# Optimization experiments

Hardware: AMD Instinct MI355X
Metric: run time of the kernel (lower is better)

## Reference

```python
import jax, jax.numpy as jnp
import numpy as np

EMA_DECAY = 0.99
LAPLACE_EPS = 1e-7
PERPLEXITY_EPS = 1e-10
COMMIT_COEF = 0.25


def setup_inputs() -> dict:
    key = jax.random.key(0)
    k1, k2, k3, k4 = jax.random.split(key, 4)
    B, C, T, H, W = 8, 256, 4, 32, 32
    n_codes = 2048
    z = jax.random.normal(k1, (B, C, T, H, W), dtype=jnp.float32)
    embeddings = jax.random.normal(k2, (n_codes, C), dtype=jnp.float32)
    N = jnp.ones((n_codes,), dtype=jnp.float32)  # state after _init_embeddings
    z_avg = jax.random.normal(k3, (n_codes, C), dtype=jnp.float32)
    k_rand = jax.random.normal(k4, (n_codes, C), dtype=jnp.float32)  # stand-in for randperm restart rows
    return {"z": z, "embeddings": embeddings, "N": N, "z_avg": z_avg, "k_rand": k_rand}


def reference(z, embeddings, N, z_avg, k_rand):
    b, c, t, h, w = z.shape
    n_codes = embeddings.shape[0]
    # rearrange 'b c t h w -> (b t h w) c'
    flat = jnp.transpose(z, (0, 2, 3, 4, 1)).reshape(-1, c)  # [Ntok, c]
    d2 = ((flat * flat).sum(axis=1, keepdims=True)
          - 2.0 * (flat @ embeddings.T)
          + (embeddings * embeddings).sum(axis=1)[None, :])  # [Ntok, n_codes]
    idx = jnp.argmin(d2, axis=1)  # [Ntok] int
    quant_flat = embeddings[idx]  # gather, [Ntok, c]
    # back to [b, c, t, h, w] (the double-rearrange in the torch code is a net permute back)
    quant = jnp.transpose(quant_flat.reshape(b, t, h, w, c), (0, 4, 1, 2, 3))
    commitment_loss = COMMIT_COEF * jnp.mean((z - jax.lax.stop_gradient(quant)) ** 2)
    embeddings_st = jax.lax.stop_gradient(quant - z) + z  # straight-through
    # EMA codebook update (one-hot scatter expressed as segment_sum)
    ones = jnp.ones(flat.shape[0], dtype=flat.dtype)
    counts = jax.ops.segment_sum(ones, idx, num_segments=n_codes)          # n_total
    encode_sum = jax.ops.segment_sum(flat, idx, num_segments=n_codes)      # [n_codes, c]
    new_N = N * EMA_DECAY + (1.0 - EMA_DECAY) * counts
    new_z_avg = z_avg * EMA_DECAY + (1.0 - EMA_DECAY) * encode_sum
    n = new_N.sum()
    weights = (new_N + LAPLACE_EPS) / (n + n_codes * LAPLACE_EPS) * n
    new_embeddings = new_z_avg / weights[:, None]
    usage = (new_N[:, None] >= 1.0).astype(flat.dtype)
    new_embeddings = new_embeddings * usage + k_rand * (1.0 - usage)
    # perplexity
    avg_probs = counts / flat.shape[0]
    perplexity = jnp.exp(-jnp.sum(avg_probs * jnp.log(avg_probs + PERPLEXITY_EPS)))
    encodings = idx.reshape(b, t, h, w)
    return embeddings_st, encodings, commitment_loss, perplexity, new_embeddings, new_N, new_z_avg
```

## Files before the change

kernel.cpp:

```cpp
#include <hip/hip_runtime.h>
#include <math.h>

#define NCODES 2048
#define CDIM   256
#define SPAT   4096
#define NTOK   32768
#define XSTR   260
#define EPI_TOK 16

#define ETILE    32
#define HALFCODE 1024
#define NTILES   (HALFCODE / ETILE)

typedef _Float16 half8  __attribute__((ext_vector_type(8)));
typedef float    f32x4  __attribute__((ext_vector_type(4)));

#define WS_ENORM  0
#define WS_COUNTS 2048
#define WS_LOSS   4096
#define WS_N      4097
#define WS_ESUM   4100
#define WS_IDX    528388
#define WS_OFF    561156
#define WS_CUR    563204
#define WS_SORT   565252
#define WS_SCODE  598020
#define WS_CAND   630788
#define WS_E16    761860
#define WS_XH     1024004

#define O_QUANT 0
#define O_ENC   8388608
#define O_LOSS  8421376
#define O_PERP  8421377
#define O_EMB   8421378
#define O_NN    8945666
#define O_ZAVG  8947714

__device__ inline void gl_lds16(const void* g, void* l) {
    __builtin_amdgcn_global_load_lds(
        (const __attribute__((address_space(1))) void*)g,
        (__attribute__((address_space(3))) void*)l, 16, 0, 0);
}

__device__ inline unsigned umn(unsigned a, unsigned b) { return a < b ? a : b; }
__device__ inline unsigned umx(unsigned a, unsigned b) { return a > b ? a : b; }
__device__ inline unsigned shflx16(unsigned v, int off) {
    return (unsigned)__shfl_xor((int)v, off, 16);
}

__global__ void k_ecvt(const float* __restrict__ emb, float* __restrict__ ws) {
    const int tid  = threadIdx.x;
    const int code = (blockIdx.x << 3) + (tid >> 5);
    const int cg   = tid & 31;
    const float* src = emb + (size_t)code * CDIM + (cg << 3);
    const float4 f0 = *(const float4*)src;
    const float4 f1 = *(const float4*)(src + 4);
    half8 h = { (_Float16)f0.x, (_Float16)f0.y, (_Float16)f0.z, (_Float16)f0.w,
                (_Float16)f1.x, (_Float16)f1.y, (_Float16)f1.z, (_Float16)f1.w };
    char* dst = (char*)(ws + WS_E16) + (size_t)code * 512 + ((cg ^ (code & 7)) << 4);
    *(half8*)dst = h;
    float s = f0.x * f0.x + f0.y * f0.y + f0.z * f0.z + f0.w * f0.w
            + f1.x * f1.x + f1.y * f1.y + f1.z * f1.z + f1.w * f1.w;
#pragma unroll
    for (int off = 16; off; off >>= 1) s += __shfl_down(s, off, 32);
    if (cg == 0) ws[WS_ENORM + code] = s;
}

__global__ __launch_bounds__(256, 3) void k_main(
    const float* __restrict__ z, float* __restrict__ ws)
{
    __shared__ half8 Es8[2][ETILE][32];

    const int tid = threadIdx.x;
    const int blk = blockIdx.x;
    const int ch  = blk & 1;
    const int tb  = blk >> 1;
    const int b   = tb >> 5;
    const int s0  = (tb & 31) * 128;
    const float* zb = z + (size_t)b * CDIM * SPAT + s0;
    const char* e16g = (const char*)(ws + WS_E16) + (size_t)ch * HALFCODE * 512;

    const int l  = tid & 63, w = tid >> 6;
    const int lr = l & 15, lg = l >> 4;

    {
        char* dst = (char*)&Es8[0][0][0];
#pragma unroll
        for (int q = 0; q < 4; ++q) {
            const int off = ((q << 2) + w) << 10;
            gl_lds16(e16g + off + (l << 4), dst + off);
        }
    }

    half8 a[2][8];
#pragma unroll
    for (int as = 0; as < 2; ++as)
#pragma unroll
    for (int ks = 0; ks < 8; ++ks) {
        float v[8];
#pragma unroll
        for (int e = 0; e < 8; ++e)
            v[e] = zb[(size_t)(ks * 32 + lg * 8 + e) * SPAT + (w * 32 + as * 16 + lr)];
        half8 h = { (_Float16)v[0], (_Float16)v[1], (_Float16)v[2], (_Float16)v[3],
                    (_Float16)v[4], (_Float16)v[5], (_Float16)v[6], (_Float16)v[7] };
        a[as][ks] = h;
    }

    if (ch == 0) {
        _Float16* xh = (_Float16*)(ws + WS_XH);
#pragma unroll
        for (int as = 0; as < 2; ++as) {
            _Float16* xr = xh + (size_t)(b * SPAT + s0 + w * 32 + as * 16 + lr) * CDIM;
#pragma unroll
            for (int ks = 0; ks < 8; ++ks)
                *(half8*)(xr + ks * 32 + lg * 8) = a[as][ks];
        }
    }

    unsigned kb0[2][4], kb1[2][4];
#pragma unroll
    for (int as = 0; as < 2; ++as)
#pragma unroll
    for (int r = 0; r < 4; ++r) { kb0[as][r] = 0xFFFFFFFFu; kb1[as][r] = 0xFFFFFFFFu; }

    __syncthreads();

    int p = 0;
    for (int tile = 0; tile < NTILES; ++tile) {
        if (tile < NTILES - 1) {
            const char* src = e16g + (size_t)(tile + 1) * (ETILE * 512);
            char* dst = (char*)&Es8[p ^ 1][0][0];
#pragma unroll
            for (int q = 0; q < 4; ++q) {
                const int off = ((q << 2) + w) << 10;
                gl_lds16(src + off + (l << 4), dst + off);
            }
        }

        const float en0 = ws[WS_ENORM + ch * HALFCODE + tile * ETILE + lr];
        const float en1 = ws[WS_ENORM + ch * HALFCODE + tile * ETILE + 16 + lr];

        f32x4 acc[2][2];
#pragma unroll
        for (int as = 0; as < 2; ++as)
#pragma unroll
        for (int j = 0; j < 2; ++j) acc[as][j] = (f32x4)0.0f;

        half8 bf0[2], bf1[2];
#pragma unroll
        for (int j = 0; j < 2; ++j) {
            const int row = j * 16 + lr;
            bf0[j] = Es8[p][row][lg ^ (row & 7)];
        }
#pragma unroll
        for (int ks = 0; ks < 8; ++ks) {
            if (ks < 7) {
#pragma unroll
                for (int j = 0; j < 2; ++j) {
                    const int row = j * 16 + lr;
                    if (ks & 1) bf0[j] = Es8[p][row][((ks + 1) * 4 + lg) ^ (row & 7)];
                    else        bf1[j] = Es8[p][row][((ks + 1) * 4 + lg) ^ (row & 7)];
                }
            }
            __builtin_amdgcn_s_setprio(1);
#pragma unroll
            for (int as = 0; as < 2; ++as)
#pragma unroll
            for (int j = 0; j < 2; ++j)
                acc[as][j] = __builtin_amdgcn_mfma_f32_16x16x32_f16(
                    a[as][ks], (ks & 1) ? bf1[j] : bf0[j], acc[as][j], 0, 0, 0);
            __builtin_amdgcn_s_setprio(0);
        }

        const float enb0 = en0 + 4096.0f;
        const float enb1 = en1 + 4096.0f;
        const unsigned code0 = (unsigned)(ch * HALFCODE + tile * ETILE + lr);
        const unsigned code1 = code0 + 16u;
#pragma unroll
        for (int as = 0; as < 2; ++as)
#pragma unroll
        for (int r = 0; r < 4; ++r) {
            {
                const float d = fmaf(acc[as][0][r], -2.0f, enb0);
                const unsigned key = (__float_as_uint(d) & 0xFFFFF800u) | code0;
                const unsigned hi = umx(kb0[as][r], key);
                kb0[as][r] = umn(kb0[as][r], key);
                kb1[as][r] = umn(kb1[as][r], hi);
            }
            {
                const float d = fmaf(acc[as][1][r], -2.0f, enb1);
                const unsigned key = (__float_as_uint(d) & 0xFFFFF800u) | code1;
                const unsigned hi = umx(kb0[as][r], key);
                kb0[as][r] = umn(kb0[as][r], key);
                kb1[as][r] = umn(kb1[as][r], hi);
            }
        }

        __syncthreads();
        p ^= 1;
    }

#pragma unroll
    for (int as = 0; as < 2; ++as)
#pragma unroll
    for (int r = 0; r < 4; ++r) {
        unsigned k0 = kb0[as][r], k1 = kb1[as][r];
        unsigned k2 = 0xFFFFFFFFu, k3 = 0xFFFFFFFFu;
#pragma unroll
        for (int off = 8; off; off >>= 1) {
            const unsigned o0 = shflx16(k0, off);
            const unsigned o1 = shflx16(k1, off);
            const unsigned o2 = shflx16(k2, off);
            const unsigned o3 = shflx16(k3, off);
            const unsigned m0 = umn(k0, o3), m1 = umn(k1, o2);
            const unsigned m2 = umn(k2, o1), m3 = umn(k3, o0);
            const unsigned t0 = umn(m0, m2), t2 = umx(m0, m2);
            const unsigned t1 = umn(m1, m3), t3 = umx(m1, m3);
            k0 = umn(t0, t1); k1 = umx(t0, t1);
            k2 = umn(t2, t3); k3 = umx(t2, t3);
        }
        if (lr == 0) {
            const int tokg = b * SPAT + s0 + w * 32 + as * 16 + lg * 4 + r;
            ushort4 c4;
            c4.x = (unsigned short)(k0 & 2047u);
            c4.y = (unsigned short)(k1 & 2047u);
            c4.z = (unsigned short)(k2 & 2047u);
            c4.w = (unsigned short)(k3 & 2047u);
            *(ushort4*)((unsigned short*)((int*)ws + WS_CAND) + (size_t)tokg * 8 + ch * 4) = c4;
        }
    }
}

__global__ __launch_bounds__(256, 6) void k_epi(
    const float* __restrict__ z, const float* __restrict__ emb,
    float* __restrict__ ws, float* __restrict__ out)
{
    __shared__ float Xs[EPI_TOK * XSTR];
    __shared__ int   idxs[EPI_TOK];
    __shared__ float lloss[EPI_TOK];

    const int tid = threadIdx.x, blk = blockIdx.x;
    const int b   = blk >> 8;
    const int s0  = (blk & 255) * EPI_TOK;
    const float* zb = z + (size_t)b * CDIM * SPAT + s0;

    {
        const int s  = tid & 15;
        const int c0 = tid >> 4;
#pragma unroll 4
        for (int c = c0; c < CDIM; c += 16)
            Xs[s * XSTR + c] = zb[(size_t)c * SPAT + s];
    }
    __syncthreads();

    {
        const int t = tid >> 4, h = tid & 15, j = h & 7;
        const unsigned short* cp =
            (const unsigned short*)((int*)ws + WS_CAND) + ((size_t)blk * EPI_TOK + t) * 8;
        const int mycand = cp[j];
        const float en_h = ws[WS_ENORM + mycand];

        int cand[8];
        {
            const ushort4 ca = *(const ushort4*)cp;
            const ushort4 cb = *(const ushort4*)(cp + 4);
            cand[0] = ca.x; cand[1] = ca.y; cand[2] = ca.z; cand[3] = ca.w;
            cand[4] = cb.x; cand[5] = cb.y; cand[6] = cb.z; cand[7] = cb.w;
        }

        float4 xq[4];
#pragma unroll
        for (int q = 0; q < 4; ++q)
            xq[q] = *(const float4*)&Xs[t * XSTR + q * 64 + h * 4];

        float xn = 0.0f;
#pragma unroll
        for (int q = 0; q < 4; ++q)
            xn += xq[q].x * xq[q].x + xq[q].y * xq[q].y
                + xq[q].z * xq[q].z + xq[q].w * xq[q].w;

        float p8[8];
#pragma unroll
        for (int k = 0; k < 8; ++k) {
            const float* er = emb + (size_t)cand[k] * CDIM + h * 4;
            float dp = 0.0f;
#pragma unroll
            for (int q = 0; q < 4; ++q) {
                const float4 e4 = *(const float4*)(er + q * 64);
                dp += xq[q].x * e4.x + xq[q].y * e4.y + xq[q].z * e4.z + xq[q].w * e4.w;
            }
            p8[k] = dp;
        }

#pragma unroll
        for (int k = 0; k < 8; ++k) p8[k] += __shfl_xor(p8[k], 8, 16);
        xn += __shfl_xor(xn, 8, 16);

        float np4[4];
#pragma unroll
        for (int k2 = 0; k2 < 4; ++k2) {
            const float own = (h & 1) ? p8[2 * k2 + 1] : p8[2 * k2];
            const float snd = (h & 1) ? p8[2 * k2]     : p8[2 * k2 + 1];
            np4[k2] = own + __shfl_xor(snd, 1, 16);
        }
        xn += __shfl_xor(xn, 1, 16);
        float nq2[2];
#pragma unroll
        for (int k3 = 0; k3 < 2; ++k3) {
            const float own = ((h >> 1) & 1) ? np4[2 * k3 + 1] : np4[2 * k3];
            const float snd = ((h >> 1) & 1) ? np4[2 * k3]     : np4[2 * k3 + 1];
            nq2[k3] = own + __shfl_xor(snd, 2, 16);
        }
        xn += __shfl_xor(xn, 2, 16);
        const float own = ((h >> 2) & 1) ? nq2[1] : nq2[0];
        const float snd = ((h >> 2) & 1) ? nq2[0] : nq2[1];
        const float dot = own + __shfl_xor(snd, 4, 16);
        xn += __shfl_xor(xn, 4, 16);

        float bd = en_h - 2.0f * dot;
        int   bi = mycand;
#pragma unroll
        for (int off = 1; off < 16; off <<= 1) {
            const float od = __shfl_xor(bd, off, 16);
            const int   oi = __shfl_xor(bi, off, 16);
            if (od < bd || (od == bd && oi < bi)) { bd = od; bi = oi; }
        }
        if (h == 0) {
            idxs[t]  = bi;
            lloss[t] = xn + bd;
            out[O_ENC + blk * EPI_TOK + t] = (float)bi;
            ((int*)ws)[WS_IDX + blk * EPI_TOK + t] = bi;
            atomicAdd(ws + WS_COUNTS + bi, 1.0f);
        }
    }
    __syncthreads();

    {
        const int t = tid >> 4, h = tid & 15;
        const float* ewin = emb + (size_t)idxs[t] * CDIM + h * 4;
#pragma unroll
        for (int q = 0; q < 4; ++q)
            *(float4*)&Xs[t * XSTR + q * 64 + h * 4] = *(const float4*)(ewin + q * 64);
    }
    __syncthreads();

    {
        const int s  = tid & 15;
        const int c0 = tid >> 4;
        float* qcol = out + O_QUANT + (size_t)b * CDIM * SPAT + s0 + s;
#pragma unroll 4
        for (int c = c0; c < CDIM; c += 16)
            qcol[(size_t)c * SPAT] = Xs[s * XSTR + c];
    }
    if (tid == 0) {
        float ls = 0.0f;
#pragma unroll
        for (int t = 0; t < EPI_TOK; ++t) ls += lloss[t];
        atomicAdd(ws + WS_LOSS, ls);
    }
}

__global__ void k_finalize(const float* __restrict__ Nin, float* __restrict__ ws,
                           float* __restrict__ out) {
    __shared__ float r1[4], r2[4];
    __shared__ int   wsum[4];
    const int tid  = threadIdx.x;
    const int base = tid * 8;

    float cnt[8];
    {
        const float4 c0 = *(const float4*)(ws + WS_COUNTS + base);
        const float4 c1 = *(const float4*)(ws + WS_COUNTS + base + 4);
        cnt[0] = c0.x; cnt[1] = c0.y; cnt[2] = c0.z; cnt[3] = c0.w;
        cnt[4] = c1.x; cnt[5] = c1.y; cnt[6] = c1.z; cnt[7] = c1.w;
    }

    float nsum = 0.0f, H = 0.0f;
    int   tsum = 0;
#pragma unroll
    for (int j = 0; j < 8; ++j) {
        const float cf = cnt[j];
        const float nn = Nin[base + j] * 0.99f + 0.01f * cf;
        out[O_NN + base + j] = nn;
        nsum += nn;
        const float p = cf * (1.0f / 32768.0f);
        H += p * logf(p + 1e-10f);
        tsum += (int)cf;
    }

    int inc = tsum;
#pragma unroll
    for (int off = 1; off < 64; off <<= 1) {
        const int v = __shfl_up(inc, off, 64);
        if ((tid & 63) >= off) inc += v;
    }
    const int wv = tid >> 6, ln = tid & 63;
    if (ln == 63) wsum[wv] = inc;

#pragma unroll
    for (int off = 32; off; off >>= 1) {
        nsum += __shfl_down(nsum, off);
        H    += __shfl_down(H, off);
    }
    if (ln == 0) { r1[wv] = nsum; r2[wv] = H; }
    __syncthreads();

    int wbase = 0;
    for (int q = 0; q < wv; ++q) wbase += wsum[q];
    int run = wbase + inc - tsum;
    int* offp = (int*)ws + WS_OFF;
    int* curp = (int*)ws + WS_CUR;
#pragma unroll
    for (int j = 0; j < 8; ++j) {
        offp[base + j] = run;
        curp[base + j] = run;
        run += (int)cnt[j];
    }

    if (tid == 0) {
        const float nt = r1[0] + r1[1] + r1[2] + r1[3];
        const float Ht = r2[0] + r2[1] + r2[2] + r2[3];
        ws[WS_N] = nt;
        out[O_PERP] = expf(-Ht);
        out[O_LOSS] = 0.25f * ws[WS_LOSS] * (1.0f / 8388608.0f);
    }
}

__global__ void k_scatter(float* __restrict__ ws) {
    const int t    = blockIdx.x * 256 + threadIdx.x;
    const int code = ((const int*)ws)[WS_IDX + t];
    const int slot = atomicAdd((int*)ws + WS_CUR + code, 1);
    ((int*)ws)[WS_SORT  + slot] = t;
    ((int*)ws)[WS_SCODE + slot] = code;
}

__global__ __launch_bounds__(256) void k_gather(float* __restrict__ ws) {
    __shared__ int stok[64], scod[64];
    const int g = blockIdx.x, tid = threadIdx.x, c = tid;
    if (tid < 64) {
        stok[tid] = ((const int*)ws)[WS_SORT  + g * 64 + tid];
        scod[tid] = ((const int*)ws)[WS_SCODE + g * 64 + tid];
    }
    __syncthreads();

    const _Float16* xh = (const _Float16*)(ws + WS_XH);
    float* esum = ws + WS_ESUM;

    float acc = 0.0f;
    for (int k0 = 0; k0 < 64; k0 += 8) {
        float v[8];
#pragma unroll
        for (int j = 0; j < 8; ++j)
            v[j] = (float)xh[(size_t)stok[k0 + j] * CDIM + c];
#pragma unroll
        for (int j = 0; j < 8; ++j) {
            const int k = k0 + j;
            acc += v[j];
            if (k == 63 || scod[k] != scod[k + 1]) {
                atomicAdd(&esum[(size_t)scod[k] * CDIM + c], acc);
                acc = 0.0f;
            }
        }
    }
}

__global__ __launch_bounds__(256) void k_update(
    const float* __restrict__ zavg, const float* __restrict__ krand,
    const float* __restrict__ ws, float* __restrict__ out)
{
    const int i = blockIdx.x, c = threadIdx.x;
    const float nn  = out[O_NN + i];
    const float n   = ws[WS_N];
    const float wgt = (nn + 1e-7f) / (n + NCODES * 1e-7f) * n;
    const size_t o  = (size_t)i * CDIM + c;
    const float ez  = 0.99f * zavg[o] + 0.01f * ws[WS_ESUM + o];
    out[O_ZAVG + o] = ez;
    out[O_EMB + o]  = (nn >= 1.0f) ? (ez / wgt) : krand[o];
}

extern "C" void kernel_launch(void* const* d_in, const int* in_sizes, int n_in,
                              void* d_out, int out_size, void* d_ws, size_t ws_size,
                              hipStream_t stream) {
    const float* z     = (const float*)d_in[0];
    const float* emb   = (const float*)d_in[1];
    const float* Nin   = (const float*)d_in[2];
    const float* zavg  = (const float*)d_in[3];
    const float* krand = (const float*)d_in[4];
    float* out = (float*)d_out;
    float* ws  = (float*)d_ws;

    hipMemsetAsync(ws + WS_COUNTS, 0,
                   (size_t)(2048 + 4 + NCODES * CDIM) * sizeof(float), stream);

    k_ecvt    <<<NCODES / 8,  256, 0, stream>>>(emb, ws);
    k_main    <<<512,         256, 0, stream>>>(z, ws);
    k_epi     <<<2048,        256, 0, stream>>>(z, emb, ws, out);
    k_finalize<<<1,           256, 0, stream>>>(Nin, ws, out);
    k_scatter <<<NTOK / 256,  256, 0, stream>>>(ws);
    k_gather  <<<NTOK / 64,   256, 0, stream>>>(ws);
    k_update  <<<NCODES,      256, 0, stream>>>(zavg, krand, ws, out);
}
```

Before: 148.3 us.

## Split codebook search into quarters across 1024 blocks with XCD-aware mapping

The fp16 MFMA nearest-code search now splits the codebook into four quarters instead of two, doubling the grid to 1024 blocks and raising launch bounds occupancy to 4. Block indices are remapped so that the four quarter-blocks for one token tile land on the same XCD, which should improve L2 reuse of the z tile. Each token now carries 16 candidate codes instead of 8, so the fp32 rescoring epilogue runs two passes and reads twice the candidate embeddings. This trades more candidate storage and epilogue work, plus a redundant reload of z by each quarter-block, for more parallelism in the main kernel.

```diff
diff --git a/kernel.cpp b/kernel.cpp
--- a/kernel.cpp
+++ b/kernel.cpp
@@ -9,8 +9,8 @@
 #define EPI_TOK 16
 
 #define ETILE    32
-#define HALFCODE 1024
-#define NTILES   (HALFCODE / ETILE)
+#define QCODE    512
+#define NTILES   (QCODE / ETILE)
 
 typedef _Float16 half8  __attribute__((ext_vector_type(8)));
 typedef float    f32x4  __attribute__((ext_vector_type(4)));
@@ -26,8 +26,8 @@
 #define WS_SORT   565252
 #define WS_SCODE  598020
 #define WS_CAND   630788
-#define WS_E16    761860
-#define WS_XH     1024004
+#define WS_E16    892932
+#define WS_XH     1155076
 
 #define O_QUANT 0
 #define O_ENC   8388608
@@ -67,19 +67,20 @@
     if (cg == 0) ws[WS_ENORM + code] = s;
 }
 
-__global__ __launch_bounds__(256, 3) void k_main(
+__global__ __launch_bounds__(256, 4) void k_main(
     const float* __restrict__ z, float* __restrict__ ws)
 {
     __shared__ half8 Es8[2][ETILE][32];
 
     const int tid = threadIdx.x;
-    const int blk = blockIdx.x;
-    const int ch  = blk & 1;
-    const int tb  = blk >> 1;
-    const int b   = tb >> 5;
-    const int s0  = (tb & 31) * 128;
+    const int raw = blockIdx.x;
+    const int xcd = raw & 7, sub = raw >> 3;
+    const int g   = xcd * 32 + (sub >> 2);
+    const int qtr = sub & 3;
+    const int b   = g >> 5;
+    const int s0  = (g & 31) * 128;
     const float* zb = z + (size_t)b * CDIM * SPAT + s0;
-    const char* e16g = (const char*)(ws + WS_E16) + (size_t)ch * HALFCODE * 512;
+    const char* e16g = (const char*)(ws + WS_E16) + (size_t)qtr * QCODE * 512;
 
     const int l  = tid & 63, w = tid >> 6;
     const int lr = l & 15, lg = l >> 4;
@@ -107,7 +108,7 @@
         a[as][ks] = h;
     }
 
-    if (ch == 0) {
+    if (qtr == 0) {
         _Float16* xh = (_Float16*)(ws + WS_XH);
 #pragma unroll
         for (int as = 0; as < 2; ++as) {
@@ -138,8 +139,8 @@
             }
         }
 
-        const float en0 = ws[WS_ENORM + ch * HALFCODE + tile * ETILE + lr];
-        const float en1 = ws[WS_ENORM + ch * HALFCODE + tile * ETILE + 16 + lr];
+        const float en0 = ws[WS_ENORM + qtr * QCODE + tile * ETILE + lr];
+        const float en1 = ws[WS_ENORM + qtr * QCODE + tile * ETILE + 16 + lr];
 
         f32x4 acc[2][2];
 #pragma unroll
@@ -175,7 +176,7 @@
 
         const float enb0 = en0 + 4096.0f;
         const float enb1 = en1 + 4096.0f;
-        const unsigned code0 = (unsigned)(ch * HALFCODE + tile * ETILE + lr);
+        const unsigned code0 = (unsigned)(qtr * QCODE + tile * ETILE + lr);
         const unsigned code1 = code0 + 16u;
 #pragma unroll
         for (int as = 0; as < 2; ++as)
@@ -227,7 +228,7 @@
             c4.y = (unsigned short)(k1 & 2047u);
             c4.z = (unsigned short)(k2 & 2047u);
             c4.w = (unsigned short)(k3 & 2047u);
-            *(ushort4*)((unsigned short*)((int*)ws + WS_CAND) + (size_t)tokg * 8 + ch * 4) = c4;
+            *(ushort4*)((unsigned short*)((int*)ws + WS_CAND) + (size_t)tokg * 16 + qtr * 4) = c4;
         }
     }
 }
@@ -257,17 +258,7 @@
     {
         const int t = tid >> 4, h = tid & 15, j = h & 7;
         const unsigned short* cp =
-            (const unsigned short*)((int*)ws + WS_CAND) + ((size_t)blk * EPI_TOK + t) * 8;
-        const int mycand = cp[j];
-        const float en_h = ws[WS_ENORM + mycand];
-
-        int cand[8];
-        {
-            const ushort4 ca = *(const ushort4*)cp;
-            const ushort4 cb = *(const ushort4*)(cp + 4);
-            cand[0] = ca.x; cand[1] = ca.y; cand[2] = ca.z; cand[3] = ca.w;
-            cand[4] = cb.x; cand[5] = cb.y; cand[6] = cb.z; cand[7] = cb.w;
-        }
+            (const unsigned short*)((int*)ws + WS_CAND) + ((size_t)blk * EPI_TOK + t) * 16;
 
         float4 xq[4];
 #pragma unroll
@@ -279,47 +270,64 @@
         for (int q = 0; q < 4; ++q)
             xn += xq[q].x * xq[q].x + xq[q].y * xq[q].y
                 + xq[q].z * xq[q].z + xq[q].w * xq[q].w;
-
-        float p8[8];
-#pragma unroll
-        for (int k = 0; k < 8; ++k) {
-            const float* er = emb + (size_t)cand[k] * CDIM + h * 4;
-            float dp = 0.0f;
-#pragma unroll
-            for (int q = 0; q < 4; ++q) {
-                const float4 e4 = *(const float4*)(er + q * 64);
-                dp += xq[q].x * e4.x + xq[q].y * e4.y + xq[q].z * e4.z + xq[q].w * e4.w;
-            }
-            p8[k] = dp;
-        }
-
-#pragma unroll
-        for (int k = 0; k < 8; ++k) p8[k] += __shfl_xor(p8[k], 8, 16);
         xn += __shfl_xor(xn, 8, 16);
-
-        float np4[4];
-#pragma unroll
-        for (int k2 = 0; k2 < 4; ++k2) {
-            const float own = (h & 1) ? p8[2 * k2 + 1] : p8[2 * k2];
-            const float snd = (h & 1) ? p8[2 * k2]     : p8[2 * k2 + 1];
-            np4[k2] = own + __shfl_xor(snd, 1, 16);
-        }
         xn += __shfl_xor(xn, 1, 16);
-        float nq2[2];
-#pragma unroll
-        for (int k3 = 0; k3 < 2; ++k3) {
-            const float own = ((h >> 1) & 1) ? np4[2 * k3 + 1] : np4[2 * k3];
-            const float snd = ((h >> 1) & 1) ? np4[2 * k3]     : np4[2 * k3 + 1];
-            nq2[k3] = own + __shfl_xor(snd, 2, 16);
-        }
         xn += __shfl_xor(xn, 2, 16);
-        const float own = ((h >> 2) & 1) ? nq2[1] : nq2[0];
-        const float snd = ((h >> 2) & 1) ? nq2[0] : nq2[1];
-        const float dot = own + __shfl_xor(snd, 4, 16);
         xn += __shfl_xor(xn, 4, 16);
 
-        float bd = en_h - 2.0f * dot;
-        int   bi = mycand;
+        float bd = 3.4e38f;
+        int   bi = 0x7fffffff;
+#pragma unroll
+        for (int pass = 0; pass < 2; ++pass) {
+            const int mycand = cp[pass * 8 + j];
+            const float en_h = ws[WS_ENORM + mycand];
+
+            int cand[8];
+            {
+                const ushort4 ca = *(const ushort4*)(cp + pass * 8);
+                const ushort4 cb = *(const ushort4*)(cp + pass * 8 + 4);
+                cand[0] = ca.x; cand[1] = ca.y; cand[2] = ca.z; cand[3] = ca.w;
+                cand[4] = cb.x; cand[5] = cb.y; cand[6] = cb.z; cand[7] = cb.w;
+            }
+
+            float p8[8];
+#pragma unroll
+            for (int k = 0; k < 8; ++k) {
+                const float* er = emb + (size_t)cand[k] * CDIM + h * 4;
+                float dp = 0.0f;
+#pragma unroll
+                for (int q = 0; q < 4; ++q) {
+                    const float4 e4 = *(const float4*)(er + q * 64);
+                    dp += xq[q].x * e4.x + xq[q].y * e4.y + xq[q].z * e4.z + xq[q].w * e4.w;
+                }
+                p8[k] = dp;
+            }
+
+#pragma unroll
+            for (int k = 0; k < 8; ++k) p8[k] += __shfl_xor(p8[k], 8, 16);
+
+            float np4[4];
+#pragma unroll
+            for (int k2 = 0; k2 < 4; ++k2) {
+                const float own = (h & 1) ? p8[2 * k2 + 1] : p8[2 * k2];
+                const float snd = (h & 1) ? p8[2 * k2]     : p8[2 * k2 + 1];
+                np4[k2] = own + __shfl_xor(snd, 1, 16);
+            }
+            float nq2[2];
+#pragma unroll
+            for (int k3 = 0; k3 < 2; ++k3) {
+                const float own = ((h >> 1) & 1) ? np4[2 * k3 + 1] : np4[2 * k3];
+                const float snd = ((h >> 1) & 1) ? np4[2 * k3]     : np4[2 * k3 + 1];
+                nq2[k3] = own + __shfl_xor(snd, 2, 16);
+            }
+            const float own = ((h >> 2) & 1) ? nq2[1] : nq2[0];
+            const float snd = ((h >> 2) & 1) ? nq2[0] : nq2[1];
+            const float dot = own + __shfl_xor(snd, 4, 16);
+
+            const float d = en_h - 2.0f * dot;
+            if (d < bd || (d == bd && mycand < bi)) { bd = d; bi = mycand; }
+        }
+
 #pragma unroll
         for (int off = 1; off < 16; off <<= 1) {
             const float od = __shfl_xor(bd, off, 16);
@@ -494,7 +502,7 @@
                    (size_t)(2048 + 4 + NCODES * CDIM) * sizeof(float), stream);
 
     k_ecvt    <<<NCODES / 8,  256, 0, stream>>>(emb, ws);
-    k_main    <<<512,         256, 0, stream>>>(z, ws);
+    k_main    <<<1024,        256, 0, stream>>>(z, ws);
     k_epi     <<<2048,        256, 0, stream>>>(z, emb, ws, out);
     k_finalize<<<1,           256, 0, stream>>>(Nin, ws, out);
     k_scatter <<<NTOK / 256,  256, 0, stream>>>(ws);
```

Measured after the change: 160.7 us. 8.4% more time.
